# Kernel tuning notes

Hardware: AMD Instinct MI355X
Metric: run time of the kernel (lower is better)

## Reference

```python
import jax, jax.numpy as jnp
import numpy as np

TIME_STEP = 3
TOPK = 84


def setup_inputs() -> dict:
    key = jax.random.key(0)
    kx, _ = jax.random.split(key)
    x = jax.random.uniform(kx, (8, 2, 352, 2048), dtype=jnp.float32)
    w = jnp.ones((), dtype=jnp.float32)
    return {"x": x, "w": w}


def reference(x, w):
    b, c, f, l = x.shape
    emb = c * TIME_STEP
    last = x[:, :, :, -1:]  # (b,c,f,1) last frame, used as right-padding
    # shift i: x[..., i:] padded on the right with i copies of the last frame
    parts = [
        x if i == 0 else jnp.concatenate(
            [x[:, :, :, i:], jnp.broadcast_to(last, (b, c, f, i))], axis=-1)
        for i in range(TIME_STEP)
    ]
    shifted = jnp.concatenate(parts, axis=1)            # (b, emb, f, l)
    shifted = shifted.transpose(0, 2, 3, 1).reshape(b, f * l, emb)  # (b, N, emb)

    query = shifted.mean(axis=1, keepdims=True)         # (b, 1, emb)
    scores = jnp.einsum('bqe,bne->bqn', query, shifted)[:, 0]  # (b, N)

    topk_scores, topk_idx = jax.lax.top_k(scores, TOPK)  # (b, K)
    vals = jnp.take_along_axis(shifted, topk_idx[:, :, None], axis=1)  # (b, K, emb)
    attn = jax.nn.softmax(topk_scores, axis=-1)          # (b, K)

    out = jnp.einsum('bk,bke->be', attn, vals) * w + query[:, 0] * (0.5 - w)  # (b, emb)
    return out.reshape(b, c, 1, TIME_STEP)
```

## Files before the change

kernel.cpp:

```cpp
#include <hip/hip_runtime.h>
#include <math.h>

#define LL 2048
#define FF 352
#define BATCH 8
#define TOPK 84
#define FPB 4
#define BPB (FF / FPB)
#define NBINS 8192
#define BINSCALE 1024.0f
#define SUBBINS 8192
#define CAP 32768
#define FCAP 1024
#define NROWS (BATCH * 2 * FF)
#define FL (FF * LL)
#define CNTSTRIDE 64

#define OFF_Q 64
#define OFF_CNT 128
#define OFF_PART 1024
#define OFF_CS 32768
#define OFF_CI 294912

__device__ __forceinline__ int coarse_bin(float sv) {
    int bin = (int)(fmaxf(sv, 0.f) * BINSCALE);
    return bin > NBINS - 1 ? NBINS - 1 : bin;
}
__device__ __forceinline__ int fine_bin(float sv, int t) {
    float f = fmaxf(sv, 0.f) * BINSCALE - (float)t;
    int s = (int)(f * (float)SUBBINS);
    s = s < 0 ? 0 : s;
    return s > SUBBINS - 1 ? SUBBINS - 1 : s;
}

__device__ __forceinline__ void find_thresh(const unsigned int* hist, int K,
                                            int tid, int lane, int wid,
                                            int* wtot, int* sres) {
    int csum = 0;
    #pragma unroll
    for (int k = 0; k < 32; ++k) csum += (int)hist[tid * 32 + ((k + tid) & 31)];
    int sfx = csum;
    #pragma unroll
    for (int d = 1; d < 64; d <<= 1) {
        int o = __shfl_down(sfx, d);
        if (lane + d < 64) sfx += o;
    }
    if (lane == 0) wtot[wid] = sfx;
    __syncthreads();
    int hi = 0;
    #pragma unroll
    for (int w2 = 0; w2 < 4; ++w2) if (w2 > wid) hi += wtot[w2];
    int SC = sfx + hi;
    int SCn = SC - csum;
    if (SC >= K && SCn < K) { sres[0] = tid; sres[1] = SCn; }
    __syncthreads();
    int cstar = sres[0], aboveC = sres[1];
    if (tid < 64) {
        int hv = (tid < 32) ? (int)hist[cstar * 32 + tid] : 0;
        int s2 = hv;
        #pragma unroll
        for (int d = 1; d < 32; d <<= 1) {
            int o = __shfl_down(s2, d);
            if (tid + d < 64) s2 += o;
        }
        int ge = aboveC + s2;
        int gt = ge - hv;
        if (tid < 32 && ge >= K && gt < K) { sres[2] = cstar * 32 + tid; sres[3] = gt; }
    }
    __syncthreads();
}

__global__ __launch_bounds__(256) void k_rowsum(const float* __restrict__ x,
                                                float* __restrict__ ws,
                                                int* __restrict__ wsi) {
    int r = blockIdx.x;
    int tid = threadIdx.x;
    if (r == 0 && tid < 8) wsi[OFF_CNT + tid * CNTSTRIDE] = 0;
    const float4* rp = (const float4*)(x + (size_t)r * LL);
    float4 v0 = rp[tid];
    float4 v1 = rp[tid + 256];
    float s = v0.x + v0.y + v0.z + v0.w + v1.x + v1.y + v1.z + v1.w;
    for (int off = 32; off; off >>= 1) s += __shfl_down(s, off);
    __shared__ float red[4];
    int lane = tid & 63, wid = tid >> 6;
    if (lane == 0) red[wid] = s;
    __syncthreads();
    float* part = ws + OFF_PART + 4 * r;
    if (tid == 0) {
        part[0] = red[0] + red[1] + red[2] + red[3];
        part[1] = v0.x;
        part[2] = v0.y;
    }
    if (tid == 255) part[3] = v1.w;
}

__global__ __launch_bounds__(256, 4) void k_score(const float* __restrict__ x,
                                                  float* __restrict__ ws,
                                                  int* __restrict__ wsi) {
    __shared__ unsigned int hist[NBINS];
    __shared__ float4 red0[4], red1[4];
    __shared__ float sq[6];
    __shared__ int wtot[4], sres[4];
    __shared__ int lcnt, lbase;
    int tid = threadIdx.x;
    int b = blockIdx.x / BPB, blk = blockIdx.x % BPB;
    int fb = blk * FPB;
    int lane = tid & 63, wid = tid >> 6;

    for (int k = 0; k < NBINS / 256; ++k) hist[tid + (k << 8)] = 0u;
    if (tid == 0) lcnt = 0;

    float4 acc0 = {0.f, 0.f, 0.f, 0.f}, acc1 = {0.f, 0.f, 0.f, 0.f};
    const float4* part = (const float4*)(ws + OFF_PART) + b * 2 * FF;
    for (int i = tid; i < 2 * FF; i += 256) {
        float4 p = part[i];
        if (i < FF) { acc0.x += p.x; acc0.y += p.y; acc0.z += p.z; acc0.w += p.w; }
        else        { acc1.x += p.x; acc1.y += p.y; acc1.z += p.z; acc1.w += p.w; }
    }
    for (int off = 32; off; off >>= 1) {
        acc0.x += __shfl_down(acc0.x, off); acc0.y += __shfl_down(acc0.y, off);
        acc0.z += __shfl_down(acc0.z, off); acc0.w += __shfl_down(acc0.w, off);
        acc1.x += __shfl_down(acc1.x, off); acc1.y += __shfl_down(acc1.y, off);
        acc1.z += __shfl_down(acc1.z, off); acc1.w += __shfl_down(acc1.w, off);
    }
    if (lane == 0) { red0[wid] = acc0; red1[wid] = acc1; }
    __syncthreads();
    if (tid == 0) {
        float A0 = 0, B0 = 0, C0 = 0, D0 = 0, A1 = 0, B1 = 0, C1 = 0, D1 = 0;
        for (int w2 = 0; w2 < 4; ++w2) {
            A0 += red0[w2].x; B0 += red0[w2].y; C0 += red0[w2].z; D0 += red0[w2].w;
            A1 += red1[w2].x; B1 += red1[w2].y; C1 += red1[w2].z; D1 += red1[w2].w;
        }
        const float inv = 1.f / (float)FL;
        sq[0] = A0 * inv;
        sq[1] = A1 * inv;
        sq[2] = (A0 - B0 + D0) * inv;
        sq[3] = (A1 - B1 + D1) * inv;
        sq[4] = (A0 - B0 - C0 + 2.f * D0) * inv;
        sq[5] = (A1 - B1 - C1 + 2.f * D1) * inv;
        if (blk == 0) for (int e = 0; e < 6; ++e) ws[OFF_Q + b * 6 + e] = sq[e];
    }
    __syncthreads();
    float q0 = sq[0], q1 = sq[1], q2 = sq[2], q3 = sq[3], q4 = sq[4], q5 = sq[5];

    float4 sreg[FPB][2];
    #pragma unroll
    for (int fr = 0; fr < FPB; ++fr) {
        int f = fb + fr;
        const float* r0 = x + ((size_t)(b * 2 + 0) * FF + f) * LL;
        const float* r1 = x + ((size_t)(b * 2 + 1) * FF + f) * LL;
        #pragma unroll
        for (int h = 0; h < 2; ++h) {
            int l0 = (h << 10) + tid * 4;
            float4 u = *(const float4*)(r0 + l0);
            float4 v = *(const float4*)(r1 + l0);
            float a4 = __shfl_down(u.x, 1), a5 = __shfl_down(u.y, 1);
            float b4 = __shfl_down(v.x, 1), b5 = __shfl_down(v.y, 1);
            if (lane == 63) {
                if (l0 == LL - 4) { a4 = u.w; a5 = u.w; b4 = v.w; b5 = v.w; }
                else { a4 = r0[l0 + 4]; a5 = r0[l0 + 5];
                       b4 = r1[l0 + 4]; b5 = r1[l0 + 5]; }
            }
            float4 s;
            s.x = q0 * u.x + q1 * v.x + q2 * u.y + q3 * v.y + q4 * u.z + q5 * v.z;
            s.y = q0 * u.y + q1 * v.y + q2 * u.z + q3 * v.z + q4 * u.w + q5 * v.w;
            s.z = q0 * u.z + q1 * v.z + q2 * u.w + q3 * v.w + q4 * a4 + q5 * b4;
            s.w = q0 * u.w + q1 * v.w + q2 * a4 + q3 * b4 + q4 * a5 + q5 * b5;
            sreg[fr][h] = s;
            #pragma unroll
            for (int j = 0; j < 4; ++j) {
                float sv = j == 0 ? s.x : (j == 1 ? s.y : (j == 2 ? s.z : s.w));
                atomicAdd(&hist[coarse_bin(sv)], 1u);
            }
        }
    }
    __syncthreads();

    find_thresh(hist, TOPK, tid, lane, wid, wtot, sres);
    int t = sres[2];

    unsigned int kmask = 0u;
    #pragma unroll
    for (int fr = 0; fr < FPB; ++fr) {
        #pragma unroll
        for (int h = 0; h < 2; ++h) {
            float4 s = sreg[fr][h];
            #pragma unroll
            for (int j = 0; j < 4; ++j) {
                float sv = j == 0 ? s.x : (j == 1 ? s.y : (j == 2 ? s.z : s.w));
                if (coarse_bin(sv) >= t) kmask |= 1u << ((fr << 3) + (h << 2) + j);
            }
        }
    }
    int cnt = __popc(kmask);
    int myoff = 0;
    if (cnt) myoff = atomicAdd(&lcnt, cnt);
    __syncthreads();
    if (tid == 0) lbase = atomicAdd(&wsi[OFF_CNT + b * CNTSTRIDE], lcnt);
    __syncthreads();
    int pos = lbase + myoff;
    #pragma unroll
    for (int fr = 0; fr < FPB; ++fr) {
        #pragma unroll
        for (int h = 0; h < 2; ++h) {
            float4 s = sreg[fr][h];
            int l0 = (h << 10) + tid * 4;
            int nb = (fb + fr) * LL + l0;
            #pragma unroll
            for (int j = 0; j < 4; ++j) {
                if (kmask & (1u << ((fr << 3) + (h << 2) + j))) {
                    float sv = j == 0 ? s.x : (j == 1 ? s.y : (j == 2 ? s.z : s.w));
                    if (pos < CAP) {
                        ws[OFF_CS + b * CAP + pos] = sv;
                        wsi[OFF_CI + b * CAP + pos] = nb + j;
                    }
                    ++pos;
                }
            }
        }
    }
}

__global__ __launch_bounds__(256) void k_final(const float* __restrict__ x,
                                               const float* __restrict__ wv,
                                               const float* __restrict__ ws,
                                               const int* __restrict__ wsi,
                                               float* __restrict__ out) {
    __shared__ union {
        unsigned int hist[NBINS];
        struct { float cs[FCAP]; int ci[FCAP]; } fin;
    } sh;
    __shared__ int wtot[4], sres[4];
    __shared__ int cnt2;
    __shared__ float redm[4];
    __shared__ float den;
    __shared__ float accsh[8];
    int tid = threadIdx.x;
    int b = blockIdx.x;
    int lane = tid & 63, wid = tid >> 6;

    int C = wsi[OFF_CNT + b * CNTSTRIDE];
    if (C > CAP) C = CAP;
    const float* gcs = ws + OFF_CS + b * CAP;
    const int* gci = wsi + OFF_CI + b * CAP;

    for (int k = 0; k < NBINS / 256; ++k) sh.hist[tid + (k << 8)] = 0u;
    __syncthreads();
    for (int p4 = tid * 4; p4 < C; p4 += 1024) {
        float4 s4 = *(const float4*)(gcs + p4);
        int lim = C - p4;
        atomicAdd(&sh.hist[coarse_bin(s4.x)], 1u);
        if (lim > 1) atomicAdd(&sh.hist[coarse_bin(s4.y)], 1u);
        if (lim > 2) atomicAdd(&sh.hist[coarse_bin(s4.z)], 1u);
        if (lim > 3) atomicAdd(&sh.hist[coarse_bin(s4.w)], 1u);
    }
    __syncthreads();
    find_thresh(sh.hist, TOPK, tid, lane, wid, wtot, sres);
    int t = sres[2];
    int above = sres[3];

    for (int k = 0; k < NBINS / 256; ++k) sh.hist[tid + (k << 8)] = 0u;
    __syncthreads();
    for (int p4 = tid * 4; p4 < C; p4 += 1024) {
        float4 s4 = *(const float4*)(gcs + p4);
        int lim = C - p4;
        #pragma unroll
        for (int j = 0; j < 4; ++j) {
            if (j >= lim) break;
            float sv = j == 0 ? s4.x : (j == 1 ? s4.y : (j == 2 ? s4.z : s4.w));
            if (coarse_bin(sv) == t) atomicAdd(&sh.hist[fine_bin(sv, t)], 1u);
        }
    }
    __syncthreads();
    find_thresh(sh.hist, TOPK - above, tid, lane, wid, wtot, sres);
    int t2 = sres[2];
    if (tid == 0) cnt2 = 0;
    __syncthreads();

    for (int p4 = tid * 4; p4 < C; p4 += 1024) {
        float4 s4 = *(const float4*)(gcs + p4);
        int4 i4 = *(const int4*)(gci + p4);
        int lim = C - p4;
        #pragma unroll
        for (int j = 0; j < 4; ++j) {
            if (j >= lim) break;
            float sv = j == 0 ? s4.x : (j == 1 ? s4.y : (j == 2 ? s4.z : s4.w));
            int iv = j == 0 ? i4.x : (j == 1 ? i4.y : (j == 2 ? i4.z : i4.w));
            int bin = coarse_bin(sv);
            bool keep = (bin > t) || (bin == t && fine_bin(sv, t) >= t2);
            if (keep) {
                int q = atomicAdd(&cnt2, 1);
                if (q < FCAP) { sh.fin.cs[q] = sv; sh.fin.ci[q] = iv; }
            }
        }
    }
    __syncthreads();
    int C2 = cnt2;
    if (C2 > FCAP) C2 = FCAP;

    if (tid < 8) accsh[tid] = 0.f;
    if (tid == 0) den = 0.f;
    __syncthreads();

    float m = -INFINITY;
    for (int p = tid; p < C2; p += 256) m = fmaxf(m, sh.fin.cs[p]);
    for (int off = 32; off; off >>= 1) m = fmaxf(m, __shfl_down(m, off));
    if (lane == 0) redm[wid] = m;
    __syncthreads();
    float smax = fmaxf(fmaxf(redm[0], redm[1]), fmaxf(redm[2], redm[3]));

    float g0 = 0.f, g1 = 0.f, g2 = 0.f, g3 = 0.f, g4 = 0.f, g5 = 0.f, dden = 0.f;
    for (int p = tid; p < C2; p += 256) {
        float s = sh.fin.cs[p];
        int idx = sh.fin.ci[p];
        int rank = 0;
        for (int j = 0; j < C2; ++j) {
            float sj = sh.fin.cs[j];
            int ij = sh.fin.ci[j];
            rank += (sj > s) || (sj == s && ij < idx);
        }
        if (rank < TOPK) {
            float pexp = expf(s - smax);
            dden += pexp;
            int f = idx >> 11, l = idx & (LL - 1);
            int l1 = l + 1 < LL ? l + 1 : LL - 1;
            int l2 = l + 2 < LL ? l + 2 : LL - 1;
            const float* r0 = x + ((size_t)(b * 2 + 0) * FF + f) * LL;
            const float* r1 = x + ((size_t)(b * 2 + 1) * FF + f) * LL;
            g0 += pexp * r0[l];
            g1 += pexp * r1[l];
            g2 += pexp * r0[l1];
            g3 += pexp * r1[l1];
            g4 += pexp * r0[l2];
            g5 += pexp * r1[l2];
        }
    }
    for (int off = 32; off; off >>= 1) {
        dden += __shfl_down(dden, off);
        g0 += __shfl_down(g0, off); g1 += __shfl_down(g1, off);
        g2 += __shfl_down(g2, off); g3 += __shfl_down(g3, off);
        g4 += __shfl_down(g4, off); g5 += __shfl_down(g5, off);
    }
    if (lane == 0) {
        atomicAdd(&den, dden);
        atomicAdd(&accsh[0], g0); atomicAdd(&accsh[1], g1);
        atomicAdd(&accsh[2], g2); atomicAdd(&accsh[3], g3);
        atomicAdd(&accsh[4], g4); atomicAdd(&accsh[5], g5);
    }
    __syncthreads();
    if (tid < 6) {
        float w = wv[0];
        float q = ws[OFF_Q + b * 6 + tid];
        out[b * 6 + tid] = (accsh[tid] / den) * w + q * (0.5f - w);
    }
}

extern "C" void kernel_launch(void* const* d_in, const int* in_sizes, int n_in,
                              void* d_out, int out_size, void* d_ws, size_t ws_size,
                              hipStream_t stream) {
    const float* x = (const float*)d_in[0];
    const float* w = (const float*)d_in[1];
    float* out = (float*)d_out;
    float* wsf = (float*)d_ws;
    int* wsi = (int*)d_ws;

    k_rowsum<<<NROWS, 256, 0, stream>>>(x, wsf, wsi);
    k_score<<<BATCH * BPB, 256, 0, stream>>>(x, wsf, wsi);
    k_final<<<BATCH, 256, 0, stream>>>(x, w, wsf, wsi, out);
}
```

Measured before the change: 118.2 us.

## Fuse final top-k selection into score kernel via last-block-done counter

Removes the separate k_final launch. Each score block increments a per-batch completion counter after a threadfence, and the last block for each batch runs the refinement histogram, exact ranking and softmax-weighted output. The query values come from shared memory instead of a workspace round trip. This saves one kernel launch and its gap, but the tail work for each batch now runs in a single trailing block of the score grid.

```diff
diff --git a/kernel.cpp b/kernel.cpp
--- a/kernel.cpp
+++ b/kernel.cpp
@@ -16,9 +16,9 @@
 #define FL (FF * LL)
 #define CNTSTRIDE 64
 
-#define OFF_Q 64
 #define OFF_CNT 128
-#define OFF_PART 1024
+#define OFF_DONE 640
+#define OFF_PART 2048
 #define OFF_CS 32768
 #define OFF_CI 294912
 
@@ -75,7 +75,10 @@
                                                 int* __restrict__ wsi) {
     int r = blockIdx.x;
     int tid = threadIdx.x;
-    if (r == 0 && tid < 8) wsi[OFF_CNT + tid * CNTSTRIDE] = 0;
+    if (r == 0 && tid < 8) {
+        wsi[OFF_CNT + tid * CNTSTRIDE] = 0;
+        wsi[OFF_DONE + tid * CNTSTRIDE] = 0;
+    }
     const float4* rp = (const float4*)(x + (size_t)r * LL);
     float4 v0 = rp[tid];
     float4 v1 = rp[tid + 256];
@@ -95,19 +98,27 @@
 }
 
 __global__ __launch_bounds__(256, 4) void k_score(const float* __restrict__ x,
+                                                  const float* __restrict__ wv,
                                                   float* __restrict__ ws,
-                                                  int* __restrict__ wsi) {
-    __shared__ unsigned int hist[NBINS];
+                                                  int* __restrict__ wsi,
+                                                  float* __restrict__ out) {
+    __shared__ union {
+        unsigned int hist[NBINS];
+        struct { float cs[FCAP]; int ci[FCAP]; } fin;
+    } sh;
     __shared__ float4 red0[4], red1[4];
     __shared__ float sq[6];
     __shared__ int wtot[4], sres[4];
-    __shared__ int lcnt, lbase;
+    __shared__ int lcnt, lbase, sIsLast, cnt2;
+    __shared__ float redm[4];
+    __shared__ float den;
+    __shared__ float accsh[8];
     int tid = threadIdx.x;
     int b = blockIdx.x / BPB, blk = blockIdx.x % BPB;
     int fb = blk * FPB;
     int lane = tid & 63, wid = tid >> 6;
 
-    for (int k = 0; k < NBINS / 256; ++k) hist[tid + (k << 8)] = 0u;
+    for (int k = 0; k < NBINS / 256; ++k) sh.hist[tid + (k << 8)] = 0u;
     if (tid == 0) lcnt = 0;
 
     float4 acc0 = {0.f, 0.f, 0.f, 0.f}, acc1 = {0.f, 0.f, 0.f, 0.f};
@@ -138,7 +149,6 @@
         sq[3] = (A1 - B1 + D1) * inv;
         sq[4] = (A0 - B0 - C0 + 2.f * D0) * inv;
         sq[5] = (A1 - B1 - C1 + 2.f * D1) * inv;
-        if (blk == 0) for (int e = 0; e < 6; ++e) ws[OFF_Q + b * 6 + e] = sq[e];
     }
     __syncthreads();
     float q0 = sq[0], q1 = sq[1], q2 = sq[2], q3 = sq[3], q4 = sq[4], q5 = sq[5];
@@ -170,13 +180,13 @@
             #pragma unroll
             for (int j = 0; j < 4; ++j) {
                 float sv = j == 0 ? s.x : (j == 1 ? s.y : (j == 2 ? s.z : s.w));
-                atomicAdd(&hist[coarse_bin(sv)], 1u);
-            }
-        }
-    }
-    __syncthreads();
-
-    find_thresh(hist, TOPK, tid, lane, wid, wtot, sres);
+                atomicAdd(&sh.hist[coarse_bin(sv)], 1u);
+            }
+        }
+    }
+    __syncthreads();
+
+    find_thresh(sh.hist, TOPK, tid, lane, wid, wtot, sres);
     int t = sres[2];
 
     unsigned int kmask = 0u;
@@ -219,25 +229,16 @@
             }
         }
     }
-}
-
-__global__ __launch_bounds__(256) void k_final(const float* __restrict__ x,
-                                               const float* __restrict__ wv,
-                                               const float* __restrict__ ws,
-                                               const int* __restrict__ wsi,
-                                               float* __restrict__ out) {
-    __shared__ union {
-        unsigned int hist[NBINS];
-        struct { float cs[FCAP]; int ci[FCAP]; } fin;
-    } sh;
-    __shared__ int wtot[4], sres[4];
-    __shared__ int cnt2;
-    __shared__ float redm[4];
-    __shared__ float den;
-    __shared__ float accsh[8];
-    int tid = threadIdx.x;
-    int b = blockIdx.x;
-    int lane = tid & 63, wid = tid >> 6;
+
+    __threadfence();
+    __syncthreads();
+    if (tid == 0) {
+        int done = atomicAdd(&wsi[OFF_DONE + b * CNTSTRIDE], 1);
+        sIsLast = (done == BPB - 1);
+    }
+    __syncthreads();
+    if (!sIsLast) return;
+    __threadfence();
 
     int C = wsi[OFF_CNT + b * CNTSTRIDE];
     if (C > CAP) C = CAP;
@@ -256,7 +257,7 @@
     }
     __syncthreads();
     find_thresh(sh.hist, TOPK, tid, lane, wid, wtot, sres);
-    int t = sres[2];
+    int t1 = sres[2];
     int above = sres[3];
 
     for (int k = 0; k < NBINS / 256; ++k) sh.hist[tid + (k << 8)] = 0u;
@@ -268,7 +269,7 @@
         for (int j = 0; j < 4; ++j) {
             if (j >= lim) break;
             float sv = j == 0 ? s4.x : (j == 1 ? s4.y : (j == 2 ? s4.z : s4.w));
-            if (coarse_bin(sv) == t) atomicAdd(&sh.hist[fine_bin(sv, t)], 1u);
+            if (coarse_bin(sv) == t1) atomicAdd(&sh.hist[fine_bin(sv, t1)], 1u);
         }
     }
     __syncthreads();
@@ -287,7 +288,7 @@
             float sv = j == 0 ? s4.x : (j == 1 ? s4.y : (j == 2 ? s4.z : s4.w));
             int iv = j == 0 ? i4.x : (j == 1 ? i4.y : (j == 2 ? i4.z : i4.w));
             int bin = coarse_bin(sv);
-            bool keep = (bin > t) || (bin == t && fine_bin(sv, t) >= t2);
+            bool keep = (bin > t1) || (bin == t1 && fine_bin(sv, t1) >= t2);
             if (keep) {
                 int q = atomicAdd(&cnt2, 1);
                 if (q < FCAP) { sh.fin.cs[q] = sv; sh.fin.ci[q] = iv; }
@@ -325,14 +326,14 @@
             int f = idx >> 11, l = idx & (LL - 1);
             int l1 = l + 1 < LL ? l + 1 : LL - 1;
             int l2 = l + 2 < LL ? l + 2 : LL - 1;
-            const float* r0 = x + ((size_t)(b * 2 + 0) * FF + f) * LL;
-            const float* r1 = x + ((size_t)(b * 2 + 1) * FF + f) * LL;
-            g0 += pexp * r0[l];
-            g1 += pexp * r1[l];
-            g2 += pexp * r0[l1];
-            g3 += pexp * r1[l1];
-            g4 += pexp * r0[l2];
-            g5 += pexp * r1[l2];
+            const float* rr0 = x + ((size_t)(b * 2 + 0) * FF + f) * LL;
+            const float* rr1 = x + ((size_t)(b * 2 + 1) * FF + f) * LL;
+            g0 += pexp * rr0[l];
+            g1 += pexp * rr1[l];
+            g2 += pexp * rr0[l1];
+            g3 += pexp * rr1[l1];
+            g4 += pexp * rr0[l2];
+            g5 += pexp * rr1[l2];
         }
     }
     for (int off = 32; off; off >>= 1) {
@@ -350,8 +351,7 @@
     __syncthreads();
     if (tid < 6) {
         float w = wv[0];
-        float q = ws[OFF_Q + b * 6 + tid];
-        out[b * 6 + tid] = (accsh[tid] / den) * w + q * (0.5f - w);
+        out[b * 6 + tid] = (accsh[tid] / den) * w + sq[tid] * (0.5f - w);
     }
 }
 
@@ -365,6 +365,5 @@
     int* wsi = (int*)d_ws;
 
     k_rowsum<<<NROWS, 256, 0, stream>>>(x, wsf, wsi);
-    k_score<<<BATCH * BPB, 256, 0, stream>>>(x, wsf, wsi);
-    k_final<<<BATCH, 256, 0, stream>>>(x, w, wsf, wsi, out);
-}
+    k_score<<<BATCH * BPB, 256, 0, stream>>>(x, w, wsf, wsi, out);
+}
```

Result: slower. 196.0 us (+65.9%).
